# Performance work log

Hardware: AMD Instinct MI355X
Metric: run time of the kernel (lower is better)

Reference implementation:

```python
import jax, jax.numpy as jnp
import numpy as np

S, B, H, D, IN = 512, 8, 8, 64, 512  # seq, batch, heads, head dim, model dim
PROJ = H * (5 * D + 2)


def setup_inputs() -> dict:
    key = jax.random.key(0)
    k0, k1, k2 = jax.random.split(key, 3)
    x = jax.random.normal(k0, (S, B, IN), jnp.float32)
    W_slow = jax.random.normal(k1, (PROJ, IN), jnp.float32) / np.sqrt(IN).astype(np.float32)
    W_out = jax.random.normal(k2, (IN, H * D), jnp.float32) / np.sqrt(H * D).astype(np.float32)
    ln_gamma = jnp.ones((IN,), jnp.float32)
    ln_beta = jnp.zeros((IN,), jnp.float32)
    return dict(x=x, W_slow=W_slow, W_out=W_out, ln_gamma=ln_gamma, ln_beta=ln_beta)


def reference(x, W_slow, W_out, ln_gamma, ln_beta):
    slen, bsz, in_dim = x.shape
    # pre-LayerNorm (torch LayerNorm: biased variance, eps=1e-5)
    mu = x.mean(-1, keepdims=True)
    var = x.var(-1, keepdims=True)
    normed = (x - mu) / jnp.sqrt(var + 1e-5) * ln_gamma + ln_beta
    qkvb = (normed @ W_slow.T).reshape(slen, bsz, H, 5 * D + 2)
    q, k, v, rk, rv, beta, rbeta = jnp.split(
        qkvb, [D, 2 * D, 3 * D, 4 * D, 5 * D, 5 * D + 1], axis=-1)
    q = jax.nn.softmax(q, axis=-1)
    k = jax.nn.softmax(k, axis=-1)
    rk = jax.nn.softmax(rk, axis=-1)
    beta = jax.nn.sigmoid(beta)    # (S,B,H,1)
    rbeta = jax.nn.sigmoid(rbeta)  # (S,B,H,1)

    # ---- fast_weight_memory: delta-rule fast weight, z_t = W_t q_t ----
    W0 = jnp.zeros((bsz, H, D, D), x.dtype)

    def fw_step(W, inp):
        qt, kt, vt, bt = inp  # (B,H,D),(B,H,D),(B,H,D),(B,H,1)
        v_old = jnp.einsum('bhij,bhj->bhi', W, kt)
        W = W + (bt * (vt - v_old))[..., :, None] * kt[..., None, :]
        z = jnp.einsum('bhij,bhj->bhi', W, qt)
        return W, z

    _, z = jax.lax.scan(fw_step, W0, (q, k, v, beta))  # z: (S,B,H,D)

    # ---- fast_rnn_v2: recurrent fast weight, h_t = z_t + R_t softmax(h_{t-1}) ----
    R0 = jnp.zeros((bsz, H, D, D), x.dtype)
    h0 = jnp.zeros((bsz, H, D), x.dtype)

    def rec_step(carry, inp):
        R, h = carry
        zt, kt, vt, bt = inp
        qh = jax.nn.softmax(h, axis=-1)
        v_old = jnp.einsum('bhij,bhj->bhi', R, kt)
        R = R + (bt * (vt - v_old))[..., :, None] * kt[..., None, :]
        h = zt + jnp.einsum('bhij,bhj->bhi', R, qh)
        return (R, h), h

    _, hs = jax.lax.scan(rec_step, (R0, h0), (z, rk, rv, rbeta))  # (S,B,H,D)

    out = hs.reshape(slen, bsz, H * D) @ W_out.T  # (S,B,IN)
    # dropout = 0.0 -> identity; residual
    return x + out
```

## Files before the change

### kernel.cpp

```cpp
#include <hip/hip_runtime.h>

#define S_LEN 512
#define BSZ 8
#define NH 8
#define HD 64
#define IN_DIM 512
#define PROJ 2576
#define SEG 322
#define AST 352
#define CHUNK 8
#define NCH 64
#define CB (CHUNK * AST * 4)

typedef __attribute__((ext_vector_type(8))) __bf16 bf16x8;
typedef __attribute__((ext_vector_type(4))) float f32x4;
typedef __attribute__((ext_vector_type(2))) float f32x2;

typedef union { f32x4 v4; f32x2 v2[2]; float f[4]; } u4;

static __device__ __forceinline__ unsigned short f2bf(float f) {
  unsigned u = __float_as_uint(f);
  unsigned r = (u + 0x7fffu + ((u >> 16) & 1u)) >> 16;
  return (unsigned short)r;
}
static __device__ __forceinline__ float bf2f(unsigned short s) {
  return __uint_as_float(((unsigned)s) << 16);
}

static __device__ __forceinline__ f32x2 pk_fma(f32x2 a, f32x2 b, f32x2 c) {
  f32x2 d;
  asm("v_pk_fma_f32 %0, %1, %2, %3" : "=v"(d) : "v"(a), "v"(b), "v"(c));
  return d;
}
static __device__ __forceinline__ f32x2 pk_add(f32x2 a, f32x2 b) {
  f32x2 d;
  asm("v_pk_add_f32 %0, %1, %2" : "=v"(d) : "v"(a), "v"(b));
  return d;
}

static __device__ __forceinline__ void gl_lds16(const void* g, void* l) {
  __builtin_amdgcn_global_load_lds(
      (const __attribute__((address_space(1))) unsigned int*)g,
      (__attribute__((address_space(3))) unsigned int*)l, 16, 0, 0);
}

__global__ __launch_bounds__(256) void ln_kernel(const float* __restrict__ x,
                                                 const float* __restrict__ gamma,
                                                 const float* __restrict__ beta,
                                                 unsigned short* __restrict__ out) {
  int wave = threadIdx.x >> 6, lane = threadIdx.x & 63;
  int row = blockIdx.x * 4 + wave;
  const float* xr = x + (size_t)row * IN_DIM + lane * 8;
  float4 a = *(const float4*)xr;
  float4 b = *(const float4*)(xr + 4);
  float vals[8] = {a.x, a.y, a.z, a.w, b.x, b.y, b.z, b.w};
  float s = 0.f, ss = 0.f;
#pragma unroll
  for (int i = 0; i < 8; i++) { s += vals[i]; ss += vals[i] * vals[i]; }
#pragma unroll
  for (int o = 32; o; o >>= 1) { s += __shfl_xor(s, o); ss += __shfl_xor(ss, o); }
  float mu = s * (1.f / 512.f);
  float var = ss * (1.f / 512.f) - mu * mu;
  float rstd = rsqrtf(var + 1e-5f);
  const float* g = gamma + lane * 8;
  const float* be = beta + lane * 8;
  float4 g1 = *(const float4*)g, g2 = *(const float4*)(g + 4);
  float4 b1 = *(const float4*)be, b2 = *(const float4*)(be + 4);
  float gs[8] = {g1.x, g1.y, g1.z, g1.w, g2.x, g2.y, g2.z, g2.w};
  float bs[8] = {b1.x, b1.y, b1.z, b1.w, b2.x, b2.y, b2.z, b2.w};
  union { unsigned short u[8]; uint4 v; } pk;
#pragma unroll
  for (int i = 0; i < 8; i++) pk.u[i] = f2bf((vals[i] - mu) * rstd * gs[i] + bs[i]);
  *(uint4*)(out + (size_t)row * IN_DIM + lane * 8) = pk.v;
}

__global__ void cast_kernel(const float* __restrict__ in, unsigned short* __restrict__ out, int n) {
  int i = blockIdx.x * blockDim.x + threadIdx.x;
  int st = gridDim.x * blockDim.x;
  for (; i < n; i += st) out[i] = f2bf(in[i]);
}

template <int BF16_OUT, int RESID>
__global__ __launch_bounds__(256) void gemm_bt(const unsigned short* __restrict__ A,
                                               const unsigned short* __restrict__ B,
                                               void* __restrict__ Cout,
                                               const float* __restrict__ resid,
                                               int M, int N, int K) {
  __shared__ __align__(16) unsigned short As[64][40];
  __shared__ __align__(16) unsigned short Bs[64][40];
  int tid = threadIdx.x;
  int lane = tid & 63, wave = tid >> 6;
  int m0 = blockIdx.y * 64, n0 = blockIdx.x * 64;
  int srow = tid >> 2, skq = (tid & 3) * 8;
  const unsigned short* Ap = A + (size_t)(m0 + srow) * K + skq;
  const unsigned short* Bp = B + (size_t)(n0 + srow) * K + skq;
  bool bvalid = (n0 + srow) < N;
  f32x4 zero = {0.f, 0.f, 0.f, 0.f};
  f32x4 acc[4];
#pragma unroll
  for (int nt = 0; nt < 4; nt++) acc[nt] = zero;
  int q = lane >> 4, m16 = lane & 15;
  for (int k0 = 0; k0 < K; k0 += 32) {
    uint4 av = *(const uint4*)(Ap + k0);
    uint4 bz = {0u, 0u, 0u, 0u};
    uint4 bv = bvalid ? *(const uint4*)(Bp + k0) : bz;
    *(uint4*)&As[srow][skq] = av;
    *(uint4*)&Bs[srow][skq] = bv;
    __syncthreads();
    bf16x8 af = *(const bf16x8*)&As[wave * 16 + m16][q * 8];
#pragma unroll
    for (int nt = 0; nt < 4; nt++) {
      bf16x8 bfv = *(const bf16x8*)&Bs[nt * 16 + m16][q * 8];
      acc[nt] = __builtin_amdgcn_mfma_f32_16x16x32_bf16(af, bfv, acc[nt], 0, 0, 0);
    }
    __syncthreads();
  }
  int rbase = q * 4;
#pragma unroll
  for (int nt = 0; nt < 4; nt++) {
#pragma unroll
    for (int rr = 0; rr < 4; rr++) {
      int gm = m0 + wave * 16 + rbase + rr;
      int gn = n0 + nt * 16 + m16;
      if (gn < N) {
        float v = acc[nt][rr];
        if (BF16_OUT) {
          ((unsigned short*)Cout)[(size_t)gm * N + gn] = f2bf(v);
        } else {
          float o = v;
          if (RESID) o += resid[(size_t)gm * N + gn];
          ((float*)Cout)[(size_t)gm * N + gn] = o;
        }
      }
    }
  }
}

__global__ __launch_bounds__(256) void act_kernel(const unsigned short* __restrict__ qkvb,
                                                  float* __restrict__ act) {
  int gw = blockIdx.x * 4 + (threadIdx.x >> 6);
  int l = threadIdx.x & 63;
  int m = gw >> 3, hh = gw & 7;
  int t = m >> 3, b = m & 7;
  const unsigned short* src = qkvb + (size_t)m * PROJ + hh * SEG;
  float fq = bf2f(src[l]);
  float fk = bf2f(src[64 + l]);
  float fv = bf2f(src[128 + l]);
  float fr = bf2f(src[192 + l]);
  float frv = bf2f(src[256 + l]);
  float mq = fq, mk = fk, mr = fr;
#pragma unroll
  for (int o = 32; o; o >>= 1) {
    mq = fmaxf(mq, __shfl_xor(mq, o));
    mk = fmaxf(mk, __shfl_xor(mk, o));
    mr = fmaxf(mr, __shfl_xor(mr, o));
  }
  float eq = __expf(fq - mq), ek = __expf(fk - mk), er = __expf(fr - mr);
  float sq = eq, sk = ek, sr = er;
#pragma unroll
  for (int o = 32; o; o >>= 1) {
    sq += __shfl_xor(sq, o);
    sk += __shfl_xor(sk, o);
    sr += __shfl_xor(sr, o);
  }
  int bh = b * 8 + hh;
  float* dst = act + ((size_t)bh * S_LEN + t) * AST;
  dst[l] = eq * __builtin_amdgcn_rcpf(sq);
  dst[64 + l] = ek * __builtin_amdgcn_rcpf(sk);
  dst[128 + l] = er * __builtin_amdgcn_rcpf(sr);
  dst[192 + l] = fv;
  dst[256 + l] = frv;
  if (l < 2) {
    float xv = bf2f(src[320 + l]);
    dst[320 + l] = __builtin_amdgcn_rcpf(1.f + __expf(-xv));
  }
}

__global__ __launch_bounds__(128, 1) void scan_kernel(const float* __restrict__ act,
                                                      unsigned short* __restrict__ hs) {
  int bh = blockIdx.x;
  int b = bh >> 3, hh = bh & 7;
  int tid = threadIdx.x, l = tid & 63, w = tid >> 6;

  __shared__ __align__(16) float stage[4][CHUNK * AST];
  __shared__ __align__(16) float zring[4][CHUNK][64];
  __shared__ __align__(16) float ehb[64];
  __shared__ int flags[16];

  volatile int* w0done = &flags[0];
  volatile int* w1done = &flags[8];

  const char* abase = (const char*)(act + (size_t)bh * S_LEN * AST);

  if (tid == 0) { flags[0] = 0; flags[8] = 0; }
  if (w) ehb[l] = 1.f;
  if (w == 0) {
#pragma unroll
    for (int i = 0; i < 11; i++)
      gl_lds16(abase + (size_t)i * 1024 + l * 16, (char*)&stage[0][0] + i * 1024);
  }
  __syncthreads();

  f32x2 M2[32];
#pragma unroll
  for (int j = 0; j < 32; j++) M2[j] = (f32x2){0.f, 0.f};
  const f32x2 zz = {0.f, 0.f};

  if (w == 0) {
    for (int c = 0; c < NCH; c++) {
      if (c >= 3) {
        while (*w1done < c - 2) __builtin_amdgcn_s_sleep(2);
      }
      if (c + 1 < NCH) {
        const char* nb = abase + (size_t)(c + 1) * CB;
        char* sb = (char*)&stage[(c + 1) & 3][0];
#pragma unroll
        for (int i = 0; i < 11; i++)
          gl_lds16(nb + (size_t)i * 1024 + l * 16, sb + i * 1024);
        asm volatile("s_waitcnt vmcnt(11)" ::: "memory");
      } else {
        asm volatile("s_waitcnt vmcnt(0)" ::: "memory");
      }
      const float* cb = &stage[c & 3][0];
      float* zc = &zring[c & 3][0][0];
#pragma unroll
      for (int s = 0; s < CHUNK; s++) {
        const float* stf = cb + s * AST;
        const f32x4* st4 = (const f32x4*)stf;
        float cv = stf[192 + l];
        float bt = stf[320];
        u4 kv[16];
#pragma unroll
        for (int j = 0; j < 16; j++) kv[j].v4 = st4[16 + j];
#pragma unroll
        for (int j = 0; j < 16; j++) asm("" : "+v"(kv[j].v4));
        f32x2 a0 = zz, a1 = zz, a2 = zz, a3 = zz;
#pragma unroll
        for (int j = 0; j < 16; j += 2) {
          a0 = pk_fma(M2[2 * j],     kv[j].v2[0],     a0);
          a1 = pk_fma(M2[2 * j + 1], kv[j].v2[1],     a1);
          a2 = pk_fma(M2[2 * j + 2], kv[j + 1].v2[0], a2);
          a3 = pk_fma(M2[2 * j + 3], kv[j + 1].v2[1], a3);
        }
        f32x2 vo = pk_add(pk_add(a0, a1), pk_add(a2, a3));
        float vold = vo.x + vo.y;
        float coef = bt * (cv - vold);
        f32x2 c2 = {coef, coef};
        a0 = a1 = a2 = a3 = zz;
#pragma unroll
        for (int j = 0; j < 16; j += 2) {
          u4 qA, qB;
          qA.v4 = st4[j];
          qB.v4 = st4[j + 1];
          M2[2 * j]     = pk_fma(c2, kv[j].v2[0],     M2[2 * j]);
          a0 = pk_fma(M2[2 * j],     qA.v2[0], a0);
          M2[2 * j + 1] = pk_fma(c2, kv[j].v2[1],     M2[2 * j + 1]);
          a1 = pk_fma(M2[2 * j + 1], qA.v2[1], a1);
          M2[2 * j + 2] = pk_fma(c2, kv[j + 1].v2[0], M2[2 * j + 2]);
          a2 = pk_fma(M2[2 * j + 2], qB.v2[0], a2);
          M2[2 * j + 3] = pk_fma(c2, kv[j + 1].v2[1], M2[2 * j + 3]);
          a3 = pk_fma(M2[2 * j + 3], qB.v2[1], a3);
        }
        vo = pk_add(pk_add(a0, a1), pk_add(a2, a3));
        zc[s * 64 + l] = vo.x + vo.y;
      }
      asm volatile("s_waitcnt lgkmcnt(0)" ::: "memory");
      *w0done = c + 1;
    }
  } else {
    unsigned short* hdst = hs + (size_t)b * 512 + hh * 64 + l;
    for (int c = 0; c < NCH; c++) {
      while (*w0done < c + 1) __builtin_amdgcn_s_sleep(2);
      const float* cb = &stage[c & 3][0];
      const float* zc = &zring[c & 3][0][0];
#pragma unroll
      for (int s = 0; s < CHUNK; s++) {
        const float* stf = cb + s * AST;
        const f32x4* st4 = (const f32x4*)stf;
        float z = zc[s * 64 + l];
        float cv = stf[256 + l];
        float rb = stf[321];
        u4 kv[16];
#pragma unroll
        for (int j = 0; j < 16; j++) kv[j].v4 = st4[32 + j];
#pragma unroll
        for (int j = 0; j < 16; j++) asm("" : "+v"(kv[j].v4));
        f32x2 a0 = zz, a1 = zz, a2 = zz, a3 = zz;
#pragma unroll
        for (int j = 0; j < 16; j += 2) {
          a0 = pk_fma(M2[2 * j],     kv[j].v2[0],     a0);
          a1 = pk_fma(M2[2 * j + 1], kv[j].v2[1],     a1);
          a2 = pk_fma(M2[2 * j + 2], kv[j + 1].v2[0], a2);
          a3 = pk_fma(M2[2 * j + 3], kv[j + 1].v2[1], a3);
        }
        f32x2 vo = pk_add(pk_add(a0, a1), pk_add(a2, a3));
        float rvold = vo.x + vo.y;
        float rcoef = rb * (cv - rvold);
        f32x2 rc2 = {rcoef, rcoef};
        const f32x4* e4 = (const f32x4*)ehb;
        f32x2 s0 = zz, s1 = zz;
        a0 = a1 = a2 = a3 = zz;
#pragma unroll
        for (int j = 0; j < 16; j += 2) {
          u4 eA, eB;
          eA.v4 = e4[j];
          eB.v4 = e4[j + 1];
          M2[2 * j]     = pk_fma(rc2, kv[j].v2[0],     M2[2 * j]);
          a0 = pk_fma(M2[2 * j],     eA.v2[0], a0);
          M2[2 * j + 1] = pk_fma(rc2, kv[j].v2[1],     M2[2 * j + 1]);
          a1 = pk_fma(M2[2 * j + 1], eA.v2[1], a1);
          M2[2 * j + 2] = pk_fma(rc2, kv[j + 1].v2[0], M2[2 * j + 2]);
          a2 = pk_fma(M2[2 * j + 2], eB.v2[0], a2);
          M2[2 * j + 3] = pk_fma(rc2, kv[j + 1].v2[1], M2[2 * j + 3]);
          a3 = pk_fma(M2[2 * j + 3], eB.v2[1], a3);
          s0 = pk_add(s0, pk_add(eA.v2[0], eA.v2[1]));
          s1 = pk_add(s1, pk_add(eB.v2[0], eB.v2[1]));
        }
        f32x2 ho = pk_add(pk_add(a0, a1), pk_add(a2, a3));
        float hp = ho.x + ho.y;
        f32x2 sv = pk_add(s0, s1);
        float sm = sv.x + sv.y;
        float h = z + hp * __builtin_amdgcn_rcpf(sm);
        hdst[(size_t)(c * CHUNK + s) * (BSZ * 512)] = f2bf(h);
        ehb[l] = __expf(h - 20.f);
      }
      asm volatile("s_waitcnt lgkmcnt(0)" ::: "memory");
      *w1done = c + 1;
    }
  }
}

extern "C" void kernel_launch(void* const* d_in, const int* in_sizes, int n_in,
                              void* d_out, int out_size, void* d_ws, size_t ws_size,
                              hipStream_t stream) {
  const float* x = (const float*)d_in[0];
  const float* W_slow = (const float*)d_in[1];
  const float* W_out = (const float*)d_in[2];
  const float* gamma = (const float*)d_in[3];
  const float* beta = (const float*)d_in[4];

  char* ws = (char*)d_ws;
  size_t off = 0;
  unsigned short* normed = (unsigned short*)(ws + off); off += (size_t)4096 * 512 * 2;
  unsigned short* Wslow_b = (unsigned short*)(ws + off); off += (size_t)PROJ * 512 * 2;
  unsigned short* Wout_b = (unsigned short*)(ws + off); off += (size_t)512 * 512 * 2;
  unsigned short* qkvb = (unsigned short*)(ws + off); off += (size_t)4096 * PROJ * 2;
  float* act = (float*)(ws + off); off += (size_t)64 * S_LEN * AST * 4;
  unsigned short* hsb = normed;

  hipLaunchKernelGGL(ln_kernel, dim3(1024), dim3(256), 0, stream, x, gamma, beta, normed);
  hipLaunchKernelGGL(cast_kernel, dim3(512), dim3(256), 0, stream, W_slow, Wslow_b, PROJ * 512);
  hipLaunchKernelGGL(cast_kernel, dim3(256), dim3(256), 0, stream, W_out, Wout_b, 512 * 512);
  hipLaunchKernelGGL((gemm_bt<1, 0>), dim3((PROJ + 63) / 64, 4096 / 64), dim3(256), 0, stream,
                     normed, Wslow_b, (void*)qkvb, (const float*)nullptr, 4096, PROJ, 512);
  hipLaunchKernelGGL(act_kernel, dim3(8192), dim3(256), 0, stream, qkvb, act);
  hipLaunchKernelGGL(scan_kernel, dim3(64), dim3(128), 0, stream, act, hsb);
  hipLaunchKernelGGL((gemm_bt<0, 1>), dim3(512 / 64, 4096 / 64), dim3(256), 0, stream,
                     hsb, Wout_b, d_out, x, 4096, 512, 512);
}
```

Before: 449.6 us.

## Use 128x128 GEMM tiles with direct global-to-LDS loads and 4x4 MFMA blocking

Replaces the 64x64 GEMM with a 128x128 tile where each wave computes a 64x64 sub-block using a 4x4 grid of MFMA accumulators. Operand tiles are copied straight from global memory into LDS through the gl_lds16 path instead of passing through registers. The aim is more reuse per loaded operand and less LDS and global traffic per MFMA. The risks are fewer blocks for the output projection (128 blocks), clamped out-of-range B rows feeding unused columns, and unpadded LDS rows that may cause bank conflicts. The scan kernel also drops some asm register barriers and reorders one statement.

```diff
diff --git a/kernel.cpp b/kernel.cpp
--- a/kernel.cpp
+++ b/kernel.cpp
@@ -81,55 +81,78 @@
 }
 
 template <int BF16_OUT, int RESID>
-__global__ __launch_bounds__(256) void gemm_bt(const unsigned short* __restrict__ A,
+__global__ __launch_bounds__(256) void gemm128(const unsigned short* __restrict__ A,
                                                const unsigned short* __restrict__ B,
                                                void* __restrict__ Cout,
                                                const float* __restrict__ resid,
                                                int M, int N, int K) {
-  __shared__ __align__(16) unsigned short As[64][40];
-  __shared__ __align__(16) unsigned short Bs[64][40];
+  __shared__ __align__(16) unsigned short As[128 * 32];
+  __shared__ __align__(16) unsigned short Bs[128 * 32];
   int tid = threadIdx.x;
-  int lane = tid & 63, wave = tid >> 6;
-  int m0 = blockIdx.y * 64, n0 = blockIdx.x * 64;
-  int srow = tid >> 2, skq = (tid & 3) * 8;
-  const unsigned short* Ap = A + (size_t)(m0 + srow) * K + skq;
-  const unsigned short* Bp = B + (size_t)(n0 + srow) * K + skq;
-  bool bvalid = (n0 + srow) < N;
-  f32x4 zero = {0.f, 0.f, 0.f, 0.f};
-  f32x4 acc[4];
-#pragma unroll
-  for (int nt = 0; nt < 4; nt++) acc[nt] = zero;
+  int lane = tid & 63, w = tid >> 6;
+  int wr = w >> 1, wc = w & 1;
+  int m0 = blockIdx.y * 128, n0 = blockIdx.x * 128;
+
+  int r0 = (w * 2) * 16 + (lane >> 2);
+  int r1 = (w * 2 + 1) * 16 + (lane >> 2);
+  int kq = (lane & 3) * 8;
+  const unsigned short* A0 = A + (size_t)(m0 + r0) * K + kq;
+  const unsigned short* A1 = A + (size_t)(m0 + r1) * K + kq;
+  int bn0 = n0 + r0; if (bn0 > N - 1) bn0 = N - 1;
+  int bn1 = n0 + r1; if (bn1 > N - 1) bn1 = N - 1;
+  const unsigned short* B0 = B + (size_t)bn0 * K + kq;
+  const unsigned short* B1 = B + (size_t)bn1 * K + kq;
+  char* asb0 = (char*)As + (w * 2) * 1024;
+  char* asb1 = (char*)As + (w * 2 + 1) * 1024;
+  char* bsb0 = (char*)Bs + (w * 2) * 1024;
+  char* bsb1 = (char*)Bs + (w * 2 + 1) * 1024;
+
+  f32x4 acc[4][4];
+#pragma unroll
+  for (int i = 0; i < 4; i++)
+#pragma unroll
+    for (int j = 0; j < 4; j++) acc[i][j] = (f32x4){0.f, 0.f, 0.f, 0.f};
+
   int q = lane >> 4, m16 = lane & 15;
   for (int k0 = 0; k0 < K; k0 += 32) {
-    uint4 av = *(const uint4*)(Ap + k0);
-    uint4 bz = {0u, 0u, 0u, 0u};
-    uint4 bv = bvalid ? *(const uint4*)(Bp + k0) : bz;
-    *(uint4*)&As[srow][skq] = av;
-    *(uint4*)&Bs[srow][skq] = bv;
+    gl_lds16(A0 + k0, asb0);
+    gl_lds16(A1 + k0, asb1);
+    gl_lds16(B0 + k0, bsb0);
+    gl_lds16(B1 + k0, bsb1);
+    asm volatile("s_waitcnt vmcnt(0)" ::: "memory");
     __syncthreads();
-    bf16x8 af = *(const bf16x8*)&As[wave * 16 + m16][q * 8];
-#pragma unroll
-    for (int nt = 0; nt < 4; nt++) {
-      bf16x8 bfv = *(const bf16x8*)&Bs[nt * 16 + m16][q * 8];
-      acc[nt] = __builtin_amdgcn_mfma_f32_16x16x32_bf16(af, bfv, acc[nt], 0, 0, 0);
-    }
+    bf16x8 af[4], bfv[4];
+#pragma unroll
+    for (int f = 0; f < 4; f++)
+      af[f] = *(const bf16x8*)&As[(wr * 64 + f * 16 + m16) * 32 + q * 8];
+#pragma unroll
+    for (int f = 0; f < 4; f++)
+      bfv[f] = *(const bf16x8*)&Bs[(wc * 64 + f * 16 + m16) * 32 + q * 8];
+#pragma unroll
+    for (int fa = 0; fa < 4; fa++)
+#pragma unroll
+      for (int fb = 0; fb < 4; fb++)
+        acc[fa][fb] = __builtin_amdgcn_mfma_f32_16x16x32_bf16(af[fa], bfv[fb], acc[fa][fb], 0, 0, 0);
     __syncthreads();
   }
-  int rbase = q * 4;
-#pragma unroll
-  for (int nt = 0; nt < 4; nt++) {
-#pragma unroll
-    for (int rr = 0; rr < 4; rr++) {
-      int gm = m0 + wave * 16 + rbase + rr;
-      int gn = n0 + nt * 16 + m16;
-      if (gn < N) {
-        float v = acc[nt][rr];
-        if (BF16_OUT) {
-          ((unsigned short*)Cout)[(size_t)gm * N + gn] = f2bf(v);
-        } else {
-          float o = v;
-          if (RESID) o += resid[(size_t)gm * N + gn];
-          ((float*)Cout)[(size_t)gm * N + gn] = o;
+
+#pragma unroll
+  for (int fa = 0; fa < 4; fa++) {
+#pragma unroll
+    for (int fb = 0; fb < 4; fb++) {
+#pragma unroll
+      for (int rr = 0; rr < 4; rr++) {
+        int gm = m0 + wr * 64 + fa * 16 + q * 4 + rr;
+        int gn = n0 + wc * 64 + fb * 16 + m16;
+        if (gn < N) {
+          float v = acc[fa][fb][rr];
+          if (BF16_OUT) {
+            ((unsigned short*)Cout)[(size_t)gm * N + gn] = f2bf(v);
+          } else {
+            float o = v;
+            if (RESID) o += resid[(size_t)gm * N + gn];
+            ((float*)Cout)[(size_t)gm * N + gn] = o;
+          }
         }
       }
     }
@@ -232,8 +255,6 @@
         u4 kv[16];
 #pragma unroll
         for (int j = 0; j < 16; j++) kv[j].v4 = st4[16 + j];
-#pragma unroll
-        for (int j = 0; j < 16; j++) asm("" : "+v"(kv[j].v4));
         f32x2 a0 = zz, a1 = zz, a2 = zz, a3 = zz;
 #pragma unroll
         for (int j = 0; j < 16; j += 2) {
@@ -283,8 +304,6 @@
         u4 kv[16];
 #pragma unroll
         for (int j = 0; j < 16; j++) kv[j].v4 = st4[32 + j];
-#pragma unroll
-        for (int j = 0; j < 16; j++) asm("" : "+v"(kv[j].v4));
         f32x2 a0 = zz, a1 = zz, a2 = zz, a3 = zz;
 #pragma unroll
         for (int j = 0; j < 16; j += 2) {
@@ -317,8 +336,8 @@
           s1 = pk_add(s1, pk_add(eB.v2[0], eB.v2[1]));
         }
         f32x2 ho = pk_add(pk_add(a0, a1), pk_add(a2, a3));
+        f32x2 sv = pk_add(s0, s1);
         float hp = ho.x + ho.y;
-        f32x2 sv = pk_add(s0, s1);
         float sm = sv.x + sv.y;
         float h = z + hp * __builtin_amdgcn_rcpf(sm);
         hdst[(size_t)(c * CHUNK + s) * (BSZ * 512)] = f2bf(h);
@@ -351,10 +370,10 @@
   hipLaunchKernelGGL(ln_kernel, dim3(1024), dim3(256), 0, stream, x, gamma, beta, normed);
   hipLaunchKernelGGL(cast_kernel, dim3(512), dim3(256), 0, stream, W_slow, Wslow_b, PROJ * 512);
   hipLaunchKernelGGL(cast_kernel, dim3(256), dim3(256), 0, stream, W_out, Wout_b, 512 * 512);
-  hipLaunchKernelGGL((gemm_bt<1, 0>), dim3((PROJ + 63) / 64, 4096 / 64), dim3(256), 0, stream,
+  hipLaunchKernelGGL((gemm128<1, 0>), dim3((PROJ + 127) / 128, 4096 / 128), dim3(256), 0, stream,
                      normed, Wslow_b, (void*)qkvb, (const float*)nullptr, 4096, PROJ, 512);
   hipLaunchKernelGGL(act_kernel, dim3(8192), dim3(256), 0, stream, qkvb, act);
   hipLaunchKernelGGL(scan_kernel, dim3(64), dim3(128), 0, stream, act, hsb);
-  hipLaunchKernelGGL((gemm_bt<0, 1>), dim3(512 / 64, 4096 / 64), dim3(256), 0, stream,
+  hipLaunchKernelGGL((gemm128<0, 1>), dim3(512 / 128, 4096 / 128), dim3(256), 0, stream,
                      hsb, Wout_b, d_out, x, 4096, 512, 512);
 }
```

After: 438.9 us. 2.4% less time.
